# Kernel tuning notes

Measured on AMD Instinct MI355X. Metric: run time of the kernel, lower is better.

## Reference

```python
import jax, jax.numpy as jnp
import numpy as np

B, TK, H = 32, 1024, 512
N = 2 * H          # hidden_dim * 2
AD = 512           # attention_dimension


def setup_inputs() -> dict:
    key = jax.random.key(0)
    ks = jax.random.split(key, 11)
    s = 0.02  # weight scale
    return {
        's_t_hat': jax.random.normal(ks[0], (B, N), jnp.float32),
        'encoder_outputs': jax.random.normal(ks[1], (B, TK, N), jnp.float32),
        'encoder_feature': jax.random.normal(ks[2], (B * TK, N), jnp.float32),
        'enc_padding_mask': jax.random.uniform(ks[3], (B, TK), jnp.float32),
        'coverage': jax.random.uniform(ks[4], (B, TK), jnp.float32),
        'r_i': jax.random.normal(ks[5], (B, TK, AD), jnp.float32),
        'W_s_w': jax.random.normal(ks[6], (N, N), jnp.float32) * s,
        'W_s_b': jax.random.normal(ks[7], (N,), jnp.float32) * s,
        'W_c_w': jax.random.normal(ks[8], (N, 1), jnp.float32) * s,
        'v_w': jax.random.normal(ks[9], (1, N), jnp.float32) * s,
        'W_r_w': jax.random.normal(ks[10], (N, AD), jnp.float32) * s,
    }


def reference(s_t_hat, encoder_outputs, encoder_feature, enc_padding_mask,
              coverage, r_i, W_s_w, W_s_b, W_c_w, v_w, W_r_w):
    b, t_k, n = encoder_outputs.shape
    # decoder feature: W_s(s_t_hat), broadcast over time
    dec_fea = s_t_hat @ W_s_w.T + W_s_b                       # [b, n]
    enc_feat = encoder_feature.reshape(b, t_k, n)             # [b, t_k, n]
    # coverage feature: W_c applied to scalar coverage per position
    cov_feat = coverage[..., None] * W_c_w[:, 0]              # [b, t_k, n]
    e = jnp.tanh(enc_feat + dec_fea[:, None, :] + cov_feat)   # [b, t_k, n]
    scores = jnp.einsum('btn,n->bt', e, v_w[0])               # [b, t_k]
    attn_ = jax.nn.softmax(scores, axis=1) * enc_padding_mask
    attn = attn_ / attn_.sum(1, keepdims=True)                # renormalized
    c_t = jnp.einsum('bt,btn->bn', attn, encoder_outputs)     # [b, n]
    coverage_new = coverage + attn                            # [b, t_k]
    # structural (LSA) branch
    Wrri = jnp.einsum('bta,na->btn', r_i, W_r_w)              # [b, t_k, n]
    e_s = jnp.tanh(Wrri + dec_fea[:, None, :])
    s2 = jnp.einsum('btn,n->bt', e_s, v_w[0])
    a_struct = (jax.nn.softmax(s2, axis=1) * enc_padding_mask)[:, None, :]  # [b,1,t_k]
    c_t_struct = jnp.einsum('bt,btn->bn', a_struct[:, 0], encoder_outputs)  # [b, n]
    return (c_t, attn, coverage_new, c_t_struct, a_struct)
```

## Files before the change

### kernel.cpp

```cpp
#include <hip/hip_runtime.h>
#include <hip/hip_bf16.h>

static constexpr int BB   = 32;
static constexpr int TKK  = 1024;
static constexpr int ND   = 1024;
static constexpr int ADIM = 512;

typedef __attribute__((ext_vector_type(8))) short bf16x8;
typedef __attribute__((ext_vector_type(4))) float f32x4;

__device__ __forceinline__ float fast_tanh(float x) {
  x = fminf(fmaxf(x, -15.f), 15.f);
  float e = __expf(2.f * x);
  return __fdividef(e - 1.f, e + 1.f);
}

__device__ __forceinline__ short f2bf(float x) {
  unsigned u = __float_as_uint(x);
  u += 0x7FFF + ((u >> 16) & 1);
  return (short)(u >> 16);
}

__device__ __forceinline__ void gload_lds16(const void* g, void* l) {
  __builtin_amdgcn_global_load_lds(
      (const __attribute__((address_space(1))) unsigned int*)g,
      (__attribute__((address_space(3))) unsigned int*)l, 16, 0, 0);
}

__global__ __launch_bounds__(256) void k_pre(const float* __restrict__ r_i,
    const float* __restrict__ Wr, short* __restrict__ rb, short* __restrict__ wb,
    const float* __restrict__ s_t_hat, const float* __restrict__ Wsw,
    const float* __restrict__ Wsb, float* __restrict__ dec) {
  size_t bid = blockIdx.x;
  if (bid < 8448) {
    const float* src;
    short* dst;
    size_t i;
    if (bid < 8192) { src = r_i; dst = rb; i = bid * 256 + threadIdx.x; }
    else            { src = Wr;  dst = wb; i = (bid - 8192) * 256 + threadIdx.x; }
    float4 a = ((const float4*)src)[2 * i];
    float4 b = ((const float4*)src)[2 * i + 1];
    bf16x8 h;
    h[0] = f2bf(a.x); h[1] = f2bf(a.y); h[2] = f2bf(a.z); h[3] = f2bf(a.w);
    h[4] = f2bf(b.x); h[5] = f2bf(b.y); h[6] = f2bf(b.z); h[7] = f2bf(b.w);
    ((bf16x8*)dst)[i] = h;
  } else {
    int db = (int)bid - 8448;
    int b  = db >> 3;
    int n0 = (db & 7) << 7;
    int w = threadIdx.x >> 6, lane = threadIdx.x & 63;
    const float4* s4 = (const float4*)(s_t_hat + (size_t)b * ND);
    float4 sv0 = s4[lane], sv1 = s4[lane + 64], sv2 = s4[lane + 128], sv3 = s4[lane + 192];
    for (int nn = 0; nn < 32; nn++) {
      int n = n0 + w * 32 + nn;
      const float4* w4 = (const float4*)(Wsw + (size_t)n * ND);
      float4 wa = w4[lane], wb2 = w4[lane + 64], wc = w4[lane + 128], wd = w4[lane + 192];
      float acc = sv0.x*wa.x + sv0.y*wa.y + sv0.z*wa.z + sv0.w*wa.w
                + sv1.x*wb2.x + sv1.y*wb2.y + sv1.z*wb2.z + sv1.w*wb2.w
                + sv2.x*wc.x + sv2.y*wc.y + sv2.z*wc.z + sv2.w*wc.w
                + sv3.x*wd.x + sv3.y*wd.y + sv3.z*wd.z + sv3.w*wd.w;
      #pragma unroll
      for (int off = 32; off; off >>= 1) acc += __shfl_down(acc, off);
      if (lane == 0) dec[b * ND + n] = acc + Wsb[n];
    }
  }
}

__global__ __launch_bounds__(256) void k_decfea(const float* __restrict__ s_t_hat,
    const float* __restrict__ Wsw, const float* __restrict__ Wsb,
    float* __restrict__ dec) {
  int b  = blockIdx.x >> 3;
  int n0 = (blockIdx.x & 7) << 7;
  int w = threadIdx.x >> 6, lane = threadIdx.x & 63;
  const float4* s4 = (const float4*)(s_t_hat + (size_t)b * ND);
  float4 sv0 = s4[lane], sv1 = s4[lane + 64], sv2 = s4[lane + 128], sv3 = s4[lane + 192];
  for (int nn = 0; nn < 32; nn++) {
    int n = n0 + w * 32 + nn;
    const float4* w4 = (const float4*)(Wsw + (size_t)n * ND);
    float4 wa = w4[lane], wb = w4[lane + 64], wc = w4[lane + 128], wd = w4[lane + 192];
    float acc = sv0.x*wa.x + sv0.y*wa.y + sv0.z*wa.z + sv0.w*wa.w
              + sv1.x*wb.x + sv1.y*wb.y + sv1.z*wb.z + sv1.w*wb.w
              + sv2.x*wc.x + sv2.y*wc.y + sv2.z*wc.z + sv2.w*wc.w
              + sv3.x*wd.x + sv3.y*wd.y + sv3.z*wd.z + sv3.w*wd.w;
    #pragma unroll
    for (int off = 32; off; off >>= 1) acc += __shfl_down(acc, off);
    if (lane == 0) dec[b * ND + n] = acc + Wsb[n];
  }
}

__global__ __launch_bounds__(256) void k_scoresA(const float* __restrict__ ef,
    const float* __restrict__ dec, const float* __restrict__ Wc,
    const float* __restrict__ vw, const float* __restrict__ cov,
    float* __restrict__ scores) {
  const int bt = blockIdx.x * 4 + (threadIdx.x >> 6);
  const int b  = bt >> 10;
  const int lane = threadIdx.x & 63;
  const float c = cov[bt];
  float s = 0.f;
  #pragma unroll
  for (int q = 0; q < 4; ++q) {
    const int col = q * 256 + lane * 4;
    float4 e = *(const float4*)(ef + (size_t)bt * ND + col);
    float4 d = *(const float4*)(dec + (size_t)b * ND + col);
    float4 w = *(const float4*)(Wc + col);
    float4 v = *(const float4*)(vw + col);
    s += v.x * fast_tanh(e.x + d.x + c * w.x)
       + v.y * fast_tanh(e.y + d.y + c * w.y)
       + v.z * fast_tanh(e.z + d.z + c * w.z)
       + v.w * fast_tanh(e.w + d.w + c * w.w);
  }
  #pragma unroll
  for (int off = 32; off; off >>= 1) s += __shfl_down(s, off);
  if (lane == 0) scores[bt] = s;
}

__global__ __launch_bounds__(256) void k_mega(const short* __restrict__ rb,
    const short* __restrict__ wb, const float* __restrict__ dec,
    const float* __restrict__ vw, float* __restrict__ part,
    const float* __restrict__ ef, const float* __restrict__ Wc,
    const float* __restrict__ cov, float* __restrict__ scores) {
  const int r3 = blockIdx.x % 3;
  const int g3 = blockIdx.x / 3;
  if (r3 == 0) {
    __shared__ __align__(16) short As[2][128 * 32];
    __shared__ __align__(16) short Bs[2][128 * 32];
    const int tid = threadIdx.x;
    const int lane = tid & 63, wv = tid >> 6;
    const int wm = wv >> 1, wn = wv & 1;
    const int g = lane >> 4, cl = lane & 15;
    const int swz = (g3 & 7) * 256 + (g3 >> 3);
    const int mchunk = swz >> 3, nchunk = swz & 7;
    const int b  = mchunk >> 3;
    const int t0 = (mchunk & 7) * 128;
    const int n0 = nchunk * 128;
    const int lrow4 = lane >> 2;
    const int sck   = ((lane & 3) ^ ((lane >> 3) & 3)) * 8;
    const short* Agbase = rb + (size_t)(b * TKK + t0) * ADIM;
    const short* Bgbase = wb + (size_t)n0 * ADIM;
    const int rdsw = (g ^ ((cl >> 1) & 3)) * 8;

    f32x4 acc[4][4];
    #pragma unroll
    for (int m = 0; m < 4; ++m)
      #pragma unroll
      for (int n = 0; n < 4; ++n) acc[m][n] = (f32x4){0.f, 0.f, 0.f, 0.f};

    auto stage = [&](int buf, int kc) {
      const int k0 = kc * 32;
      #pragma unroll
      for (int p = 0; p < 2; ++p) {
        const int rowc = p * 64 + wv * 16;
        const int row  = rowc + lrow4;
        gload_lds16(Agbase + (size_t)row * ADIM + k0 + sck, &As[buf][rowc * 32]);
        gload_lds16(Bgbase + (size_t)row * ADIM + k0 + sck, &Bs[buf][rowc * 32]);
      }
    };

    stage(0, 0);
    for (int kc = 0; kc < 16; ++kc) {
      const int cur = kc & 1;
      if (kc < 15) {
        stage(cur ^ 1, kc + 1);
        asm volatile("s_waitcnt vmcnt(4)" ::: "memory");
      } else {
        asm volatile("s_waitcnt vmcnt(0)" ::: "memory");
      }
      __builtin_amdgcn_s_barrier();
      bf16x8 af[4], bfr[4];
      #pragma unroll
      for (int m = 0; m < 4; ++m)
        af[m] = *(const bf16x8*)&As[cur][(wm * 64 + m * 16 + cl) * 32 + rdsw];
      #pragma unroll
      for (int n = 0; n < 4; ++n)
        bfr[n] = *(const bf16x8*)&Bs[cur][(wn * 64 + n * 16 + cl) * 32 + rdsw];
      #pragma unroll
      for (int m = 0; m < 4; ++m)
        #pragma unroll
        for (int n = 0; n < 4; ++n)
          acc[m][n] = __builtin_amdgcn_mfma_f32_16x16x32_bf16(af[m], bfr[n], acc[m][n], 0, 0, 0);
      __builtin_amdgcn_s_barrier();
    }

    float vvv[4], ddd[4];
    #pragma unroll
    for (int n = 0; n < 4; ++n) {
      const int col = n0 + wn * 64 + n * 16 + cl;
      vvv[n] = vw[col];
      ddd[n] = dec[b * ND + col];
    }
    #pragma unroll
    for (int m = 0; m < 4; ++m) {
      #pragma unroll
      for (int r = 0; r < 4; ++r) {
        float s = 0.f;
        #pragma unroll
        for (int n = 0; n < 4; ++n)
          s += vvv[n] * fast_tanh(acc[m][n][r] + ddd[n]);
        #pragma unroll
        for (int off = 1; off < 16; off <<= 1) s += __shfl_xor(s, off);
        if (cl == 0) {
          const int rowg = b * TKK + t0 + wm * 64 + m * 16 + g * 4 + r;
          part[(size_t)rowg * 16 + nchunk * 2 + wn] = s;
        }
      }
    }
  } else {
    const int sidx = 2 * g3 + (r3 - 1);
    const int bt0 = sidx * 8 + (threadIdx.x >> 6) * 2;
    const int lane = threadIdx.x & 63;
    const int b0 = bt0 >> 10, b1 = (bt0 + 1) >> 10;
    const float c0 = cov[bt0], c1 = cov[bt0 + 1];
    float s0 = 0.f, s1 = 0.f;
    #pragma unroll
    for (int q = 0; q < 4; ++q) {
      const int col = q * 256 + lane * 4;
      float4 e0 = *(const float4*)(ef + (size_t)bt0 * ND + col);
      float4 e1 = *(const float4*)(ef + (size_t)(bt0 + 1) * ND + col);
      float4 d0 = *(const float4*)(dec + (size_t)b0 * ND + col);
      float4 d1 = *(const float4*)(dec + (size_t)b1 * ND + col);
      float4 w = *(const float4*)(Wc + col);
      float4 v = *(const float4*)(vw + col);
      s0 += v.x * fast_tanh(e0.x + d0.x + c0 * w.x)
          + v.y * fast_tanh(e0.y + d0.y + c0 * w.y)
          + v.z * fast_tanh(e0.z + d0.z + c0 * w.z)
          + v.w * fast_tanh(e0.w + d0.w + c0 * w.w);
      s1 += v.x * fast_tanh(e1.x + d1.x + c1 * w.x)
          + v.y * fast_tanh(e1.y + d1.y + c1 * w.y)
          + v.z * fast_tanh(e1.z + d1.z + c1 * w.z)
          + v.w * fast_tanh(e1.w + d1.w + c1 * w.w);
    }
    #pragma unroll
    for (int off = 32; off; off >>= 1) {
      s0 += __shfl_down(s0, off);
      s1 += __shfl_down(s1, off);
    }
    if (lane == 0) {
      scores[bt0]     = s0;
      scores[bt0 + 1] = s1;
    }
  }
}

__global__ __launch_bounds__(256) void k_gemmB(const float* __restrict__ r_i,
    const float* __restrict__ Wr, const float* __restrict__ dec,
    const float* __restrict__ vw, float* __restrict__ part) {
  __shared__ short As[128 * 64];
  __shared__ short Bs[128 * 64];
  const int tid = threadIdx.x;
  const int lane = tid & 63, wv = tid >> 6;
  const int wm = wv >> 1, wn = wv & 1;
  const int g = lane >> 4, cl = lane & 15;
  const int mchunk = blockIdx.x, nchunk = blockIdx.y;
  const int b  = mchunk >> 3;
  const int t0 = (mchunk & 7) * 128;
  const int n0 = nchunk * 128;
  const float* Ag = r_i + (size_t)(b * TKK + t0) * ADIM;
  const float* Bg = Wr + (size_t)n0 * ADIM;
  const int srow = tid >> 3, skk = (tid & 7) * 8;

  f32x4 acc[4][4];
  #pragma unroll
  for (int m = 0; m < 4; ++m)
    #pragma unroll
    for (int n = 0; n < 4; ++n) acc[m][n] = (f32x4){0.f, 0.f, 0.f, 0.f};

  for (int kc = 0; kc < 8; ++kc) {
    const int k0 = kc * 64;
    __syncthreads();
    #pragma unroll
    for (int dit = 0; dit < 4; ++dit) {
      const int row = dit * 32 + srow;
      const float* sa = Ag + (size_t)row * ADIM + k0 + skk;
      float4 a0 = *(const float4*)sa, a1 = *(const float4*)(sa + 4);
      bf16x8 ha;
      ha[0]=f2bf(a0.x); ha[1]=f2bf(a0.y); ha[2]=f2bf(a0.z); ha[3]=f2bf(a0.w);
      ha[4]=f2bf(a1.x); ha[5]=f2bf(a1.y); ha[6]=f2bf(a1.z); ha[7]=f2bf(a1.w);
      *(bf16x8*)&As[row * 64 + skk] = ha;
      const float* sbp = Bg + (size_t)row * ADIM + k0 + skk;
      float4 b0 = *(const float4*)sbp, b1 = *(const float4*)(sbp + 4);
      bf16x8 hb;
      hb[0]=f2bf(b0.x); hb[1]=f2bf(b0.y); hb[2]=f2bf(b0.z); hb[3]=f2bf(b0.w);
      hb[4]=f2bf(b1.x); hb[5]=f2bf(b1.y); hb[6]=f2bf(b1.z); hb[7]=f2bf(b1.w);
      *(bf16x8*)&Bs[row * 64 + skk] = hb;
    }
    __syncthreads();
    #pragma unroll
    for (int kf = 0; kf < 2; ++kf) {
      bf16x8 af[4], bfr[4];
      #pragma unroll
      for (int m = 0; m < 4; ++m)
        af[m] = *(const bf16x8*)&As[(wm * 64 + m * 16 + cl) * 64 + kf * 32 + g * 8];
      #pragma unroll
      for (int n = 0; n < 4; ++n)
        bfr[n] = *(const bf16x8*)&Bs[(wn * 64 + n * 16 + cl) * 64 + kf * 32 + g * 8];
      #pragma unroll
      for (int m = 0; m < 4; ++m)
        #pragma unroll
        for (int n = 0; n < 4; ++n)
          acc[m][n] = __builtin_amdgcn_mfma_f32_16x16x32_bf16(af[m], bfr[n], acc[m][n], 0, 0, 0);
    }
  }
  float vvv[4], ddd[4];
  #pragma unroll
  for (int n = 0; n < 4; ++n) {
    const int col = n0 + wn * 64 + n * 16 + cl;
    vvv[n] = vw[col];
    ddd[n] = dec[b * ND + col];
  }
  #pragma unroll
  for (int m = 0; m < 4; ++m) {
    #pragma unroll
    for (int r = 0; r < 4; ++r) {
      float s = 0.f;
      #pragma unroll
      for (int n = 0; n < 4; ++n)
        s += vvv[n] * fast_tanh(acc[m][n][r] + ddd[n]);
      #pragma unroll
      for (int off = 1; off < 16; off <<= 1) s += __shfl_xor(s, off);
      if (cl == 0) {
        const int rowg = b * TKK + t0 + wm * 64 + m * 16 + g * 4 + r;
        part[(size_t)rowg * 16 + nchunk * 2 + wn] = s;
      }
    }
  }
}

__global__ __launch_bounds__(256) void k_softmaxAB(const float* __restrict__ scores,
    const float* __restrict__ part, const float* __restrict__ mask,
    const float* __restrict__ cov, float* __restrict__ attn,
    float* __restrict__ covnew, float* __restrict__ astruct) {
  __shared__ float sb[4];
  int tid = threadIdx.x;
  if (blockIdx.x < 32) {
    int b = blockIdx.x;
    float4 s = *(const float4*)(scores + (size_t)b * TKK + tid * 4);
    float m = fmaxf(fmaxf(s.x, s.y), fmaxf(s.z, s.w));
    #pragma unroll
    for (int off = 32; off; off >>= 1) m = fmaxf(m, __shfl_down(m, off));
    if ((tid & 63) == 0) sb[tid >> 6] = m;
    __syncthreads();
    m = fmaxf(fmaxf(sb[0], sb[1]), fmaxf(sb[2], sb[3]));
    float4 mk = *(const float4*)(mask + (size_t)b * TKK + tid * 4);
    float4 e;
    e.x = __expf(s.x - m) * mk.x;
    e.y = __expf(s.y - m) * mk.y;
    e.z = __expf(s.z - m) * mk.z;
    e.w = __expf(s.w - m) * mk.w;
    float sum = e.x + e.y + e.z + e.w;
    #pragma unroll
    for (int off = 32; off; off >>= 1) sum += __shfl_down(sum, off);
    __syncthreads();
    if ((tid & 63) == 0) sb[tid >> 6] = sum;
    __syncthreads();
    float inv = __fdividef(1.f, sb[0] + sb[1] + sb[2] + sb[3]);
    float4 a = {e.x * inv, e.y * inv, e.z * inv, e.w * inv};
    *(float4*)(attn + (size_t)b * TKK + tid * 4) = a;
    float4 c = *(const float4*)(cov + (size_t)b * TKK + tid * 4);
    float4 cn = {c.x + a.x, c.y + a.y, c.z + a.z, c.w + a.w};
    *(float4*)(covnew + (size_t)b * TKK + tid * 4) = cn;
  } else {
    int b = blockIdx.x - 32;
    float sv[4];
    #pragma unroll
    for (int tt = 0; tt < 4; ++tt) {
      const float4* pp = (const float4*)(part + ((size_t)b * TKK + tid * 4 + tt) * 16);
      float4 q0 = pp[0], q1 = pp[1], q2 = pp[2], q3 = pp[3];
      sv[tt] = q0.x+q0.y+q0.z+q0.w + q1.x+q1.y+q1.z+q1.w
             + q2.x+q2.y+q2.z+q2.w + q3.x+q3.y+q3.z+q3.w;
    }
    float m = fmaxf(fmaxf(sv[0], sv[1]), fmaxf(sv[2], sv[3]));
    #pragma unroll
    for (int off = 32; off; off >>= 1) m = fmaxf(m, __shfl_down(m, off));
    if ((tid & 63) == 0) sb[tid >> 6] = m;
    __syncthreads();
    m = fmaxf(fmaxf(sb[0], sb[1]), fmaxf(sb[2], sb[3]));
    float e0 = __expf(sv[0] - m), e1 = __expf(sv[1] - m);
    float e2 = __expf(sv[2] - m), e3 = __expf(sv[3] - m);
    float sum = e0 + e1 + e2 + e3;
    #pragma unroll
    for (int off = 32; off; off >>= 1) sum += __shfl_down(sum, off);
    __syncthreads();
    if ((tid & 63) == 0) sb[tid >> 6] = sum;
    __syncthreads();
    float inv = __fdividef(1.f, sb[0] + sb[1] + sb[2] + sb[3]);
    float4 mk = *(const float4*)(mask + (size_t)b * TKK + tid * 4);
    float4 a = {e0 * mk.x * inv, e1 * mk.y * inv, e2 * mk.z * inv, e3 * mk.w * inv};
    *(float4*)(astruct + (size_t)b * TKK + tid * 4) = a;
  }
}

__global__ __launch_bounds__(256) void k_ctx(const float* __restrict__ enc,
    const float* __restrict__ attn, const float* __restrict__ astr,
    float* __restrict__ partials) {
  int tc = blockIdx.x, b = blockIdx.y;
  int tid = threadIdx.x, lane = tid & 63;
  const float4* e4 = (const float4*)(enc + (size_t)(b * TKK + tc * 32) * ND);
  float a1v = attn[(size_t)b * TKK + tc * 32 + (lane & 31)];
  float a2v = astr[(size_t)b * TKK + tc * 32 + (lane & 31)];
  float4 ac = {0, 0, 0, 0}, as = {0, 0, 0, 0};
  #pragma unroll 8
  for (int m = 0; m < 32; m++) {
    float a1 = __shfl(a1v, m), a2 = __shfl(a2v, m);
    float4 ev = e4[(size_t)m * 256 + tid];
    ac.x += a1 * ev.x; ac.y += a1 * ev.y; ac.z += a1 * ev.z; ac.w += a1 * ev.w;
    as.x += a2 * ev.x; as.y += a2 * ev.y; as.z += a2 * ev.z; as.w += a2 * ev.w;
  }
  float* p = partials + (size_t)(b * 32 + tc) * 2 * ND;
  *(float4*)(p + tid * 4) = ac;
  *(float4*)(p + ND + tid * 4) = as;
}

__global__ __launch_bounds__(256) void k_reduce(const float* __restrict__ partials,
    float* __restrict__ ct, float* __restrict__ cts) {
  int b = blockIdx.x, cx = blockIdx.y;
  int col = cx * 256 + threadIdx.x;
  float sc = 0.f, ss = 0.f;
  for (int tc = 0; tc < 32; tc++) {
    const float* p = partials + (size_t)(b * 32 + tc) * 2 * ND;
    sc += p[col];
    ss += p[ND + col];
  }
  ct[(size_t)b * ND + col] = sc;
  cts[(size_t)b * ND + col] = ss;
}

extern "C" void kernel_launch(void* const* d_in, const int* in_sizes, int n_in,
                              void* d_out, int out_size, void* d_ws, size_t ws_size,
                              hipStream_t stream) {
  const float* s_t_hat = (const float*)d_in[0];
  const float* enc_out  = (const float*)d_in[1];
  const float* enc_feat = (const float*)d_in[2];
  const float* mask     = (const float*)d_in[3];
  const float* cov      = (const float*)d_in[4];
  const float* r_i      = (const float*)d_in[5];
  const float* Wsw      = (const float*)d_in[6];
  const float* Wsb      = (const float*)d_in[7];
  const float* Wc       = (const float*)d_in[8];
  const float* vw       = (const float*)d_in[9];
  const float* Wr       = (const float*)d_in[10];

  float* out    = (float*)d_out;
  float* ct     = out;
  float* attn   = out + 32768;
  float* covnew = out + 65536;
  float* cts    = out + 98304;
  float* astr   = out + 131072;

  float* ws       = (float*)d_ws;
  float* dec      = ws;
  float* scores   = ws + 32768;
  float* s2part   = ws + 65536;
  float* partials = ws + 589824;
  short* rb       = (short*)(ws + 2686976);
  short* wb       = rb + 16777216;
  const size_t NEEDED = 2686976ull * 4 + 16777216ull * 2 + 524288ull * 2;

  if (ws_size >= NEEDED) {
    k_pre<<<8704, 256, 0, stream>>>(r_i, Wr, rb, wb, s_t_hat, Wsw, Wsb, dec);
    k_mega<<<6144, 256, 0, stream>>>(rb, wb, dec, vw, s2part,
                                     enc_feat, Wc, cov, scores);
  } else {
    k_decfea<<<256, 256, 0, stream>>>(s_t_hat, Wsw, Wsb, dec);
    k_scoresA<<<8192, 256, 0, stream>>>(enc_feat, dec, Wc, vw, cov, scores);
    k_gemmB<<<dim3(256, 8), 256, 0, stream>>>(r_i, Wr, dec, vw, s2part);
  }
  k_softmaxAB<<<64, 256, 0, stream>>>(scores, s2part, mask, cov, attn, covnew, astr);
  k_ctx<<<dim3(32, BB), 256, 0, stream>>>(enc_out, attn, astr, partials);
  k_reduce<<<dim3(BB, 4), 256, 0, stream>>>(partials, ct, cts);
}
```

Measured before the change: 164.0 us.

## Split GEMM over K halves, write raw GEMM output, move tanh-reduce into softmax

The fused GEMM blocks now split the K=512 reduction into two halves, use a three-stage LDS pipeline, and store raw fp32 accumulators for each half into a large workspace instead of applying tanh and v-reduction in the epilogue. The structural softmax kernel then re-reads both halves per row, adds dec, applies tanh and reduces with v before the softmax. This aims to raise GEMM block count and pipeline depth, but it writes and re-reads about 256 MB of intermediates and puts the tanh work into only 32 blocks, which risks a large slowdown.

```diff
diff --git a/kernel.cpp b/kernel.cpp
--- a/kernel.cpp
+++ b/kernel.cpp
@@ -119,24 +119,26 @@
     const float* __restrict__ vw, float* __restrict__ part,
     const float* __restrict__ ef, const float* __restrict__ Wc,
     const float* __restrict__ cov, float* __restrict__ scores) {
-  const int r3 = blockIdx.x % 3;
-  const int g3 = blockIdx.x / 3;
-  if (r3 == 0) {
-    __shared__ __align__(16) short As[2][128 * 32];
-    __shared__ __align__(16) short Bs[2][128 * 32];
+  if ((blockIdx.x & 1) == 0) {
+    const int gid = blockIdx.x >> 1;
+    __shared__ __align__(16) short As[3][128 * 32];
+    __shared__ __align__(16) short Bs[3][128 * 32];
     const int tid = threadIdx.x;
     const int lane = tid & 63, wv = tid >> 6;
     const int wm = wv >> 1, wn = wv & 1;
     const int g = lane >> 4, cl = lane & 15;
-    const int swz = (g3 & 7) * 256 + (g3 >> 3);
-    const int mchunk = swz >> 3, nchunk = swz & 7;
+    const int swz = (gid & 7) * 512 + (gid >> 3);
+    const int mchunk = swz >> 4;
+    const int nchunk = (swz >> 1) & 7;
+    const int kh     = swz & 1;
     const int b  = mchunk >> 3;
     const int t0 = (mchunk & 7) * 128;
     const int n0 = nchunk * 128;
+    const int kbase = kh * 256;
     const int lrow4 = lane >> 2;
     const int sck   = ((lane & 3) ^ ((lane >> 3) & 3)) * 8;
-    const short* Agbase = rb + (size_t)(b * TKK + t0) * ADIM;
-    const short* Bgbase = wb + (size_t)n0 * ADIM;
+    const short* Agbase = rb + (size_t)(b * TKK + t0) * ADIM + kbase;
+    const short* Bgbase = wb + (size_t)n0 * ADIM + kbase;
     const int rdsw = (g ^ ((cl >> 1) & 3)) * 8;
 
     f32x4 acc[4][4];
@@ -157,15 +159,18 @@
     };
 
     stage(0, 0);
-    for (int kc = 0; kc < 16; ++kc) {
-      const int cur = kc & 1;
-      if (kc < 15) {
-        stage(cur ^ 1, kc + 1);
+    stage(1, 1);
+    for (int kc = 0; kc < 8; ++kc) {
+      if (kc < 6) {
+        stage((kc + 2) % 3, kc + 2);
+        asm volatile("s_waitcnt vmcnt(8)" ::: "memory");
+      } else if (kc == 6) {
         asm volatile("s_waitcnt vmcnt(4)" ::: "memory");
       } else {
         asm volatile("s_waitcnt vmcnt(0)" ::: "memory");
       }
       __builtin_amdgcn_s_barrier();
+      const int cur = kc % 3;
       bf16x8 af[4], bfr[4];
       #pragma unroll
       for (int m = 0; m < 4; ++m)
@@ -181,31 +186,26 @@
       __builtin_amdgcn_s_barrier();
     }
 
-    float vvv[4], ddd[4];
-    #pragma unroll
-    for (int n = 0; n < 4; ++n) {
-      const int col = n0 + wn * 64 + n * 16 + cl;
-      vvv[n] = vw[col];
-      ddd[n] = dec[b * ND + col];
-    }
     #pragma unroll
     for (int m = 0; m < 4; ++m) {
       #pragma unroll
       for (int r = 0; r < 4; ++r) {
-        float s = 0.f;
+      }
+    }
+    #pragma unroll
+    for (int m = 0; m < 4; ++m) {
+      #pragma unroll
+      for (int r = 0; r < 4; ++r) {
+        const int rowg = b * TKK + t0 + wm * 64 + m * 16 + g * 4 + r;
         #pragma unroll
-        for (int n = 0; n < 4; ++n)
-          s += vvv[n] * fast_tanh(acc[m][n][r] + ddd[n]);
-        #pragma unroll
-        for (int off = 1; off < 16; off <<= 1) s += __shfl_xor(s, off);
-        if (cl == 0) {
-          const int rowg = b * TKK + t0 + wm * 64 + m * 16 + g * 4 + r;
-          part[(size_t)rowg * 16 + nchunk * 2 + wn] = s;
+        for (int n = 0; n < 4; ++n) {
+          const int col = n0 + wn * 64 + n * 16 + cl;
+          part[(size_t)rowg * (2 * ND) + kh * ND + col] = acc[m][n][r];
         }
       }
     }
   } else {
-    const int sidx = 2 * g3 + (r3 - 1);
+    const int sidx = blockIdx.x >> 1;
     const int bt0 = sidx * 8 + (threadIdx.x >> 6) * 2;
     const int lane = threadIdx.x & 63;
     const int b0 = bt0 >> 10, b1 = (bt0 + 1) >> 10;
@@ -319,17 +319,20 @@
       for (int off = 1; off < 16; off <<= 1) s += __shfl_xor(s, off);
       if (cl == 0) {
         const int rowg = b * TKK + t0 + wm * 64 + m * 16 + g * 4 + r;
-        part[(size_t)rowg * 16 + nchunk * 2 + wn] = s;
-      }
-    }
-  }
-}
-
+        part[(size_t)rowg * (2 * ND) + ND + nchunk * 2 + wn] = s;
+      }
+    }
+  }
+}
+
+template <int FASTB>
 __global__ __launch_bounds__(256) void k_softmaxAB(const float* __restrict__ scores,
     const float* __restrict__ part, const float* __restrict__ mask,
-    const float* __restrict__ cov, float* __restrict__ attn,
+    const float* __restrict__ cov, const float* __restrict__ dec,
+    const float* __restrict__ vw, float* __restrict__ attn,
     float* __restrict__ covnew, float* __restrict__ astruct) {
   __shared__ float sb[4];
+  __shared__ float srow[1024];
   int tid = threadIdx.x;
   if (blockIdx.x < 32) {
     int b = blockIdx.x;
@@ -361,12 +364,44 @@
   } else {
     int b = blockIdx.x - 32;
     float sv[4];
-    #pragma unroll
-    for (int tt = 0; tt < 4; ++tt) {
-      const float4* pp = (const float4*)(part + ((size_t)b * TKK + tid * 4 + tt) * 16);
-      float4 q0 = pp[0], q1 = pp[1], q2 = pp[2], q3 = pp[3];
-      sv[tt] = q0.x+q0.y+q0.z+q0.w + q1.x+q1.y+q1.z+q1.w
-             + q2.x+q2.y+q2.z+q2.w + q3.x+q3.y+q3.z+q3.w;
+    if (FASTB) {
+      for (int tt = 0; tt < 4; ++tt) {
+        const int row = (tid >> 6) + 4 * ((tid & 63) >> 6);
+      }
+      const int lane = tid & 63, wvv = tid >> 6;
+      for (int r0 = wvv; r0 < TKK; r0 += 4) {
+        const size_t rowg = (size_t)b * TKK + r0;
+        const float* cp = part + rowg * (2 * ND);
+        float s = 0.f;
+        #pragma unroll
+        for (int q = 0; q < 4; ++q) {
+          const int col = q * 256 + lane * 4;
+          float4 p0 = *(const float4*)(cp + col);
+          float4 p1 = *(const float4*)(cp + ND + col);
+          float4 d  = *(const float4*)(dec + (size_t)b * ND + col);
+          float4 v  = *(const float4*)(vw + col);
+          s += v.x * fast_tanh(p0.x + p1.x + d.x)
+             + v.y * fast_tanh(p0.y + p1.y + d.y)
+             + v.z * fast_tanh(p0.z + p1.z + d.z)
+             + v.w * fast_tanh(p0.w + p1.w + d.w);
+        }
+        #pragma unroll
+        for (int off = 32; off; off >>= 1) s += __shfl_down(s, off);
+        if (lane == 0) srow[r0] = s;
+      }
+      __syncthreads();
+      sv[0] = srow[tid * 4 + 0];
+      sv[1] = srow[tid * 4 + 1];
+      sv[2] = srow[tid * 4 + 2];
+      sv[3] = srow[tid * 4 + 3];
+    } else {
+      #pragma unroll
+      for (int tt = 0; tt < 4; ++tt) {
+        const float* pp = part + ((size_t)b * TKK + tid * 4 + tt) * (2 * ND) + ND;
+        float s = 0.f;
+        for (int q = 0; q < 16; ++q) s += pp[q];
+        sv[tt] = s;
+      }
     }
     float m = fmaxf(fmaxf(sv[0], sv[1]), fmaxf(sv[2], sv[3]));
     #pragma unroll
@@ -449,22 +484,26 @@
   float* ws       = (float*)d_ws;
   float* dec      = ws;
   float* scores   = ws + 32768;
-  float* s2part   = ws + 65536;
-  float* partials = ws + 589824;
-  short* rb       = (short*)(ws + 2686976);
+  float* cpart    = ws + 65536;
+  float* partials = cpart + 67108864;
+  short* rb       = (short*)(partials + 2097152);
   short* wb       = rb + 16777216;
-  const size_t NEEDED = 2686976ull * 4 + 16777216ull * 2 + 524288ull * 2;
+  const size_t NEEDED = ((size_t)32768 + 32768 + 67108864 + 2097152) * 4
+                      + (16777216ull + 524288ull) * 2;
 
   if (ws_size >= NEEDED) {
     k_pre<<<8704, 256, 0, stream>>>(r_i, Wr, rb, wb, s_t_hat, Wsw, Wsb, dec);
-    k_mega<<<6144, 256, 0, stream>>>(rb, wb, dec, vw, s2part,
+    k_mega<<<8192, 256, 0, stream>>>(rb, wb, dec, vw, cpart,
                                      enc_feat, Wc, cov, scores);
+    k_softmaxAB<1><<<64, 256, 0, stream>>>(scores, cpart, mask, cov, dec, vw,
+                                           attn, covnew, astr);
   } else {
     k_decfea<<<256, 256, 0, stream>>>(s_t_hat, Wsw, Wsb, dec);
     k_scoresA<<<8192, 256, 0, stream>>>(enc_feat, dec, Wc, vw, cov, scores);
-    k_gemmB<<<dim3(256, 8), 256, 0, stream>>>(r_i, Wr, dec, vw, s2part);
-  }
-  k_softmaxAB<<<64, 256, 0, stream>>>(scores, s2part, mask, cov, attn, covnew, astr);
+    k_gemmB<<<dim3(256, 8), 256, 0, stream>>>(r_i, Wr, dec, vw, cpart);
+    k_softmaxAB<0><<<64, 256, 0, stream>>>(scores, cpart, mask, cov, dec, vw,
+                                           attn, covnew, astr);
+  }
   k_ctx<<<dim3(32, BB), 256, 0, stream>>>(enc_out, attn, astr, partials);
   k_reduce<<<dim3(BB, 4), 256, 0, stream>>>(partials, ct, cts);
 }
```

Result: slower. 624.6 us (+280.8%).
